# Performance work log

Hardware: AMD Instinct MI355X
Metric: run time of the kernel (lower is better)

Reference implementation:

```python
import jax, jax.numpy as jnp
import numpy as np

NV = 10           # int(0.5 // 0.05), clamped to [2, 1000]
STEP = 0.05
HALF_V = 0.5
EPS = 1e-8


def _normalize(x):
    return x / (jnp.linalg.norm(x, axis=-1, keepdims=True) + EPS)


def _bilinear(img, uv):
    # img: [3, H, W]; uv: [N, 2] normalized to [0, 1). align_corners=False convention.
    C, H, W = img.shape
    x = uv[:, 0] * W - 0.5
    y = uv[:, 1] * H - 0.5
    x0 = jnp.floor(x); y0 = jnp.floor(y)
    wx = x - x0; wy = y - y0
    x0i = jnp.clip(x0.astype(jnp.int32), 0, W - 1)
    x1i = jnp.clip(x0i + 1, 0, W - 1)
    y0i = jnp.clip(y0.astype(jnp.int32), 0, H - 1)
    y1i = jnp.clip(y0i + 1, 0, H - 1)
    g = lambda yi, xi: img[:, yi, xi].T  # [N, 3]
    return (g(y0i, x0i) * ((1 - wx) * (1 - wy))[:, None]
            + g(y0i, x1i) * (wx * (1 - wy))[:, None]
            + g(y1i, x0i) * ((1 - wx) * wy)[:, None]
            + g(y1i, x1i) * (wx * wy)[:, None])


def _forward(edge_points, rgb1, rgb2, intrinsic1, intrinsic2, extrinsic1, extrinsic2, nh):
    # nh: concrete numpy int64 [E] of per-edge horizontal sample counts (non-differentiable).
    start = edge_points[:, 0]
    cur_dir = edge_points[:, 1] - start
    next_dir = edge_points[:, 3] - edge_points[:, 1]
    prev_dir = edge_points[:, 0] - edge_points[:, 2]
    cur_length = jnp.linalg.norm(cur_dir + 1e-6, axis=1)
    cur_dir = cur_dir / cur_length[:, None]
    cur_normal = _normalize(jnp.cross(cur_dir, next_dir))
    flip = cur_normal[:, 2] > 0  # dot with (0,0,1) > 0 -> flip sign
    cur_normal = jnp.where(flip[:, None], -cur_normal, cur_normal)
    cur_up = _normalize(jnp.cross(cur_normal, cur_dir))
    prev_normal = _normalize(jnp.cross(prev_dir, cur_dir))

    # ragged per-edge horizontal coordinates via cumsum offsets + repeat_interleave
    begin = np.concatenate([np.zeros(1, np.int64), np.cumsum(nh)[:-1]])
    total_x = int(nh.sum())
    dx = jnp.arange(total_x) - jnp.asarray(np.repeat(begin, nh))
    dx = dx / jnp.asarray(np.repeat(nh - 1, nh)) * jnp.repeat(cur_length, nh, total_repeat_length=total_x)
    dy = jnp.arange(NV) / (NV - 1) * HALF_V  # [NV]
    coords_x = jnp.repeat(dx, NV)            # [total_x * NV]
    coords_y = jnp.tile(dy, total_x)         # [total_x * NV]
    npe = nh * NV
    total = total_x * NV
    pts = (jnp.repeat(cur_dir, npe, axis=0, total_repeat_length=total) * coords_x[:, None]
           + jnp.repeat(cur_up, npe, axis=0, total_repeat_length=total) * coords_y[:, None]
           + jnp.repeat(start, npe, axis=0, total_repeat_length=total))  # [total, 3]

    # project into image 1
    proj1 = pts @ intrinsic1.T
    uv1 = jnp.clip(proj1[:, :2] / proj1[:, 2:3], 0.0, 0.999999)
    s1 = _bilinear(rgb1[0], uv1)

    # project into image 2 via relative transform
    K2h = jnp.eye(4, dtype=pts.dtype).at[:3, :3].set(intrinsic2)
    transform = K2h @ extrinsic2 @ jnp.linalg.inv(extrinsic1)
    pts_h = jnp.concatenate([pts, jnp.ones((pts.shape[0], 1), pts.dtype)], axis=1)
    proj2 = pts_h @ transform.T
    uv2 = jnp.clip(proj2[:, :2] / proj2[:, 2:3], 0.0, 0.999999)
    s2 = _bilinear(rgb2[0], uv2)

    similarity_loss = jnp.mean((s1 - s2) ** 2)
    normal_loss = jnp.mean(1 - jnp.sum(cur_normal * prev_normal, axis=1)) / 2
    observing_normal = _normalize(jnp.cross(edge_points[:, 0], edge_points[:, 1]))
    snp = jnp.minimum(jnp.abs(jnp.sum(cur_up * observing_normal, axis=1)), 0.5)
    normalization_loss = jnp.mean(1 - snp / 0.5)
    return similarity_loss, normal_loss, normalization_loss


def setup_inputs():
    key = jax.random.key(0)
    k0, k1, k2 = jax.random.split(key, 3)
    E = 4000
    ep = jax.random.normal(k0, (E, 4, 3), dtype=jnp.float32) * 1.5
    ep = ep.at[..., 2].add(10.0)  # camera-space points in front of the camera
    rgb1 = jax.random.uniform(k1, (1, 3, 2000, 3000), dtype=jnp.float32)
    rgb2 = jax.random.uniform(k2, (1, 3, 2000, 3000), dtype=jnp.float32)
    K = jnp.array([[0.3, 0.0, 0.5], [0.0, 0.45, 0.5], [0.0, 0.0, 1.0]], jnp.float32)
    E1 = jnp.eye(4, dtype=jnp.float32)
    E2 = jnp.eye(4, dtype=jnp.float32).at[0, 3].set(-0.5)
    return {"edge_points": ep, "rgb1": rgb1, "rgb2": rgb2,
            "intrinsic1": K, "intrinsic2": K, "extrinsic1": E1, "extrinsic2": E2}


def reference(edge_points, rgb1, rgb2, intrinsic1, intrinsic2, extrinsic1, extrinsic2):
    # num_horizontal is an integer count (no gradient in torch either): compute concretely.
    cur_len = np.asarray(jnp.linalg.norm(edge_points[:, 1] - edge_points[:, 0] + 1e-6, axis=1))
    nh = np.clip((cur_len // STEP).astype(np.int64), 2, 1000)
    return _forward(edge_points, rgb1, rgb2, intrinsic1, intrinsic2, extrinsic1, extrinsic2, nh)
```

## Files before the change

### kernel.cpp

```cpp
#include <hip/hip_runtime.h>


constexpr int NVS   = 10;
constexpr int IMG_H = 2000;
constexpr int IMG_W = 3000;
constexpr int NPIX  = IMG_H * IMG_W;
constexpr int QROW  = IMG_W / 4;
constexpr int SAMPLE_BLOCKS = 2048;
constexpr unsigned CHUNK = 512;

typedef float    fx4 __attribute__((ext_vector_type(4)));
typedef unsigned ux4 __attribute__((ext_vector_type(4)));

struct Geom {
    float p0x, p0y, p0z;
    float p1x, p1y, p1z;
    float p2x, p2y, p2z;
    float p3x, p3y, p3z;
    float cdx, cdy, cdz;
    float cnx, cny, cnz;
    float cux, cuy, cuz;
    float len;
    int   nh;
};

__device__ __forceinline__ Geom compute_geom(const float* __restrict__ ep, int e) {
    Geom g;
    const float* p = ep + (size_t)e * 12;
    g.p0x = p[0];  g.p0y = p[1];  g.p0z = p[2];
    g.p1x = p[3];  g.p1y = p[4];  g.p1z = p[5];
    g.p2x = p[6];  g.p2y = p[7];  g.p2z = p[8];
    g.p3x = p[9];  g.p3y = p[10]; g.p3z = p[11];

    float dx = g.p1x - g.p0x, dy = g.p1y - g.p0y, dz = g.p1z - g.p0z;
    float ax = dx + 1e-6f, ay = dy + 1e-6f, az = dz + 1e-6f;
    g.len = sqrtf(ax * ax + ay * ay + az * az);
    g.cdx = dx / g.len; g.cdy = dy / g.len; g.cdz = dz / g.len;

    float ndx = g.p3x - g.p1x, ndy = g.p3y - g.p1y, ndz = g.p3z - g.p1z;
    float cnx = g.cdy * ndz - g.cdz * ndy;
    float cny = g.cdz * ndx - g.cdx * ndz;
    float cnz = g.cdx * ndy - g.cdy * ndx;
    float n1 = sqrtf(cnx * cnx + cny * cny + cnz * cnz) + 1e-8f;
    cnx /= n1; cny /= n1; cnz /= n1;
    if (cnz > 0.f) { cnx = -cnx; cny = -cny; cnz = -cnz; }
    g.cnx = cnx; g.cny = cny; g.cnz = cnz;

    float cux = cny * g.cdz - cnz * g.cdy;
    float cuy = cnz * g.cdx - cnx * g.cdz;
    float cuz = cnx * g.cdy - cny * g.cdx;
    float n2 = sqrtf(cux * cux + cuy * cuy + cuz * cuz) + 1e-8f;
    g.cux = cux / n2; g.cuy = cuy / n2; g.cuz = cuz / n2;

    int nh = (int)floorf(g.len / 0.05f);
    g.nh = nh < 2 ? 2 : (nh > 1000 ? 1000 : nh);
    return g;
}

__device__ __forceinline__ double block_reduce_d(double v) {
    __shared__ double sh[256];
    int tid = threadIdx.x;
    sh[tid] = v;
    __syncthreads();
    for (int s = 128; s > 0; s >>= 1) {
        if (tid < s) sh[tid] += sh[tid + s];
        __syncthreads();
    }
    double r = sh[0];
    __syncthreads();
    return r;
}

__global__ __launch_bounds__(256) void edge_kernel(
        const float* __restrict__ ep, int E,
        double* __restrict__ normal_part,
        double* __restrict__ norz_part,
        fx4* __restrict__ geom_out,
        int* __restrict__ nh_out) {
    int e = blockIdx.x * blockDim.x + threadIdx.x;
    double t1 = 0.0, t2 = 0.0;
    if (e < E) {
        Geom g = compute_geom(ep, e);
        float pdx = g.p0x - g.p2x, pdy = g.p0y - g.p2y, pdz = g.p0z - g.p2z;
        float pnx = pdy * g.cdz - pdz * g.cdy;
        float pny = pdz * g.cdx - pdx * g.cdz;
        float pnz = pdx * g.cdy - pdy * g.cdx;
        float n = sqrtf(pnx * pnx + pny * pny + pnz * pnz) + 1e-8f;
        pnx /= n; pny /= n; pnz /= n;
        float dotn = g.cnx * pnx + g.cny * pny + g.cnz * pnz;
        t1 = (double)(1.0f - dotn);

        float ox = g.p0y * g.p1z - g.p0z * g.p1y;
        float oy = g.p0z * g.p1x - g.p0x * g.p1z;
        float oz = g.p0x * g.p1y - g.p0y * g.p1x;
        float no = sqrtf(ox * ox + oy * oy + oz * oz) + 1e-8f;
        ox /= no; oy /= no; oz /= no;
        float snp = fminf(fabsf(g.cux * ox + g.cuy * oy + g.cuz * oz), 0.5f);
        t2 = (double)(1.0f - snp / 0.5f);

        fx4 f0 = {g.cdx, g.cdy, g.cdz, g.len};
        fx4 f1 = {g.cux, g.cuy, g.cuz, 1.0f / (float)(g.nh - 1)};
        fx4 f2 = {g.p0x, g.p0y, g.p0z, 0.f};
        geom_out[e * 3 + 0] = f0;
        geom_out[e * 3 + 1] = f1;
        geom_out[e * 3 + 2] = f2;
        nh_out[e] = g.nh;
    }
    double s1 = block_reduce_d(t1);
    double s2 = block_reduce_d(t2);
    if (threadIdx.x == 0) {
        normal_part[blockIdx.x] = s1;
        norz_part[blockIdx.x]   = s2;
    }
}

__global__ __launch_bounds__(256) void prep_kernel(
        const int* __restrict__ nh, int E, unsigned* __restrict__ cum,
        const float* __restrict__ K2, const float* __restrict__ E1,
        const float* __restrict__ E2, float* __restrict__ tf) {
    __shared__ unsigned ssum[256];
    int tid = threadIdx.x;
    int K = (E + 255) / 256;
    int base = tid * K;

    unsigned s = 0;
    for (int k = 0; k < K; ++k) {
        int idx = base + k;
        if (idx < E) s += (unsigned)(nh[idx] * NVS);
    }
    ssum[tid] = s;
    __syncthreads();
    for (int off = 1; off < 256; off <<= 1) {
        unsigned add = (tid >= off) ? ssum[tid - off] : 0u;
        __syncthreads();
        ssum[tid] += add;
        __syncthreads();
    }
    unsigned run = ssum[tid] - s;
    for (int k = 0; k < K; ++k) {
        int idx = base + k;
        if (idx < E) {
            run += (unsigned)(nh[idx] * NVS);
            cum[idx + 1] = run;
        }
    }
    if (tid == 0) {
        cum[0] = 0;

        double a[4][8];
        for (int r = 0; r < 4; ++r)
            for (int c = 0; c < 4; ++c) {
                a[r][c] = (double)E1[r * 4 + c];
                a[r][4 + c] = (r == c) ? 1.0 : 0.0;
            }
        for (int col = 0; col < 4; ++col) {
            int piv = col; double best = fabs(a[col][col]);
            for (int r = col + 1; r < 4; ++r) {
                double t = fabs(a[r][col]);
                if (t > best) { best = t; piv = r; }
            }
            if (piv != col)
                for (int c = 0; c < 8; ++c) { double t = a[col][c]; a[col][c] = a[piv][c]; a[piv][c] = t; }
            double d = a[col][col];
            for (int c = 0; c < 8; ++c) a[col][c] /= d;
            for (int r = 0; r < 4; ++r) {
                if (r == col) continue;
                double f = a[r][col];
                for (int c = 0; c < 8; ++c) a[r][c] -= f * a[col][c];
            }
        }
        double inv1[4][4];
        for (int r = 0; r < 4; ++r)
            for (int c = 0; c < 4; ++c) inv1[r][c] = a[r][4 + c];

        double k2h[4][4];
        for (int r = 0; r < 4; ++r)
            for (int c = 0; c < 4; ++c) k2h[r][c] = (r == c) ? 1.0 : 0.0;
        for (int r = 0; r < 3; ++r)
            for (int c = 0; c < 3; ++c) k2h[r][c] = (double)K2[r * 3 + c];

        double m1[4][4];
        for (int r = 0; r < 4; ++r)
            for (int c = 0; c < 4; ++c) {
                double sm = 0.0;
                for (int k = 0; k < 4; ++k) sm += (double)E2[r * 4 + k] * inv1[k][c];
                m1[r][c] = sm;
            }
        for (int r = 0; r < 4; ++r)
            for (int c = 0; c < 4; ++c) {
                double sm = 0.0;
                for (int k = 0; k < 4; ++k) sm += k2h[r][k] * m1[k][c];
                tf[r * 4 + c] = (float)sm;
            }
    }
}

__device__ __forceinline__ unsigned p565(float r, float g, float b) {
    unsigned ri = (unsigned)__float2int_rn(r * 31.0f) & 31u;
    unsigned gi = (unsigned)__float2int_rn(g * 63.0f) & 63u;
    unsigned bi = (unsigned)__float2int_rn(b * 31.0f) & 31u;
    return ri | (gi << 5) | (bi << 11);
}

__global__ __launch_bounds__(256) void repack_kernel(
        const float* __restrict__ img1, const float* __restrict__ img2,
        unsigned* __restrict__ o1, unsigned* __restrict__ o2) {
    const int nq = NPIX / 4;
    int idx = blockIdx.x * blockDim.x + threadIdx.x;
    bool act = idx < 2 * nq;

    const float* img = img1;
    unsigned* out = o1;
    int q = 0;
    unsigned h0 = 0, h1 = 0, h2 = 0, h3 = 0;
    fx4 r{}, g{}, b{};

    if (act) {
        if (idx < nq) { img = img1; out = o1; q = idx; }
        else          { img = img2; out = o2; q = idx - nq; }
        r = __builtin_nontemporal_load(reinterpret_cast<const fx4*>(img) + q);
        g = __builtin_nontemporal_load(reinterpret_cast<const fx4*>(img + NPIX) + q);
        b = __builtin_nontemporal_load(reinterpret_cast<const fx4*>(img + 2 * (size_t)NPIX) + q);
        h0 = p565(r.x, g.x, b.x);
        h1 = p565(r.y, g.y, b.y);
        h2 = p565(r.z, g.z, b.z);
        h3 = p565(r.w, g.w, b.w);
    }

    unsigned h4s = __shfl_down(h0, 1, 64);

    if (act) {
        int qrow = q % QROW;
        unsigned h4;
        if (qrow == QROW - 1) {
            h4 = h3;
        } else if ((threadIdx.x & 63) == 63) {
            int nx = q * 4 + 4;
            h4 = p565(img[nx], img[NPIX + nx], img[2 * (size_t)NPIX + nx]);
        } else {
            h4 = h4s;
        }
        ux4 o;
        o.x = h0 | (h1 << 16);
        o.y = h1 | (h2 << 16);
        o.z = h2 | (h3 << 16);
        o.w = h3 | (h4 << 16);
        reinterpret_cast<ux4*>(out)[q] = o;
    }
}

__device__ __forceinline__ void sample565(const unsigned* __restrict__ img,
                                          float u, float v,
                                          float& r, float& g, float& b) {
    float x = u * (float)IMG_W - 0.5f;
    float y = v * (float)IMG_H - 0.5f;
    float x0 = floorf(x), y0 = floorf(y);
    float wx = x - x0, wy = y - y0;
    int x0i = (int)x0; x0i = x0i < 0 ? 0 : (x0i > IMG_W - 1 ? IMG_W - 1 : x0i);
    int y0i = (int)y0; y0i = y0i < 0 ? 0 : (y0i > IMG_H - 1 ? IMG_H - 1 : y0i);
    int y1i = y0i + 1; y1i = y1i > IMG_H - 1 ? IMG_H - 1 : y1i;

    unsigned t0 = img[(size_t)y0i * IMG_W + x0i];
    unsigned t1 = img[(size_t)y1i * IMG_W + x0i];

    float w00 = (1.f - wx) * (1.f - wy);
    float w10 = wx * (1.f - wy);
    float w01 = (1.f - wx) * wy;
    float w11 = wx * wy;

    r = w00 * (float)(t0 & 31u)         + w10 * (float)((t0 >> 16) & 31u)
      + w01 * (float)(t1 & 31u)         + w11 * (float)((t1 >> 16) & 31u);
    g = w00 * (float)((t0 >> 5) & 63u)  + w10 * (float)((t0 >> 21) & 63u)
      + w01 * (float)((t1 >> 5) & 63u)  + w11 * (float)((t1 >> 21) & 63u);
    b = w00 * (float)((t0 >> 11) & 31u) + w10 * (float)(t0 >> 27)
      + w01 * (float)((t1 >> 11) & 31u) + w11 * (float)(t1 >> 27);
}

__device__ __forceinline__ void bilinear3(const float* __restrict__ img,
                                          float u, float v,
                                          float& r, float& g, float& b) {
    float x = u * (float)IMG_W - 0.5f;
    float y = v * (float)IMG_H - 0.5f;
    float x0 = floorf(x), y0 = floorf(y);
    float wx = x - x0, wy = y - y0;
    int x0i = (int)x0; x0i = x0i < 0 ? 0 : (x0i > IMG_W - 1 ? IMG_W - 1 : x0i);
    int x1i = x0i + 1; x1i = x1i > IMG_W - 1 ? IMG_W - 1 : x1i;
    int y0i = (int)y0; y0i = y0i < 0 ? 0 : (y0i > IMG_H - 1 ? IMG_H - 1 : y0i);
    int y1i = y0i + 1; y1i = y1i > IMG_H - 1 ? IMG_H - 1 : y1i;
    float w00 = (1.f - wx) * (1.f - wy);
    float w10 = wx * (1.f - wy);
    float w01 = (1.f - wx) * wy;
    float w11 = wx * wy;
    float out[3];
#pragma unroll
    for (int c = 0; c < 3; ++c) {
        const float* p = img + (size_t)c * NPIX;
        float v00 = p[(size_t)y0i * IMG_W + x0i];
        float v10 = p[(size_t)y0i * IMG_W + x1i];
        float v01 = p[(size_t)y1i * IMG_W + x0i];
        float v11 = p[(size_t)y1i * IMG_W + x1i];
        out[c] = v00 * w00 + v10 * w10 + v01 * w01 + v11 * w11;
    }
    r = out[0]; g = out[1]; b = out[2];
}

__device__ __forceinline__ int find_edge(const unsigned* __restrict__ cum,
                                         int E, unsigned s) {
    int lo = 0, hi = E - 1;
    while (lo < hi) {
        int mid = (lo + hi + 1) >> 1;
        if (cum[mid] <= s) lo = mid; else hi = mid - 1;
    }
    return lo;
}

template <bool PACKED>
__global__ __launch_bounds__(256) void sample_kernel_t(
        const fx4* __restrict__ geom,
        const unsigned* __restrict__ cum, int E,
        const void* __restrict__ vimg1,
        const void* __restrict__ vimg2,
        const float* __restrict__ K1,
        const float* __restrict__ tf,
        double* __restrict__ sim_part) {
    __shared__ int sh_ea[2], sh_eb[2];
    int tid = threadIdx.x;

    unsigned NS = cum[E];
    unsigned nch = (NS + CHUNK - 1u) / CHUNK;

    float k00 = K1[0], k01 = K1[1], k02 = K1[2];
    float k10 = K1[3], k11 = K1[4], k12 = K1[5];
    float k20 = K1[6], k21 = K1[7], k22 = K1[8];
    float t00 = tf[0],  t01 = tf[1],  t02 = tf[2],  t03 = tf[3];
    float t10 = tf[4],  t11 = tf[5],  t12 = tf[6],  t13 = tf[7];
    float t20 = tf[8],  t21 = tf[9],  t22 = tf[10], t23 = tf[11];

    const unsigned* img1 = (const unsigned*)vimg1;
    const unsigned* img2 = (const unsigned*)vimg2;
    const float* fimg1 = (const float*)vimg1;
    const float* fimg2 = (const float*)vimg2;

    const float INV31 = 1.0f / 31.0f;
    const float INV63 = 1.0f / 63.0f;

    double lsum = 0.0;
    int it = 0;

    auto sample_one = [&](unsigned s, int e) {
        while (e + 1 < E && cum[e + 1] <= s) ++e;
        unsigned q = s - cum[e];
        int i = (int)(q / (unsigned)NVS);
        int j = (int)(q - (unsigned)(i * NVS));

        fx4 f0 = geom[e * 3 + 0];
        fx4 f1 = geom[e * 3 + 1];
        fx4 f2 = geom[e * 3 + 2];

        float dxv = ((float)i * f1.w) * f0.w;
        float dyv = ((float)j / 9.0f) * 0.5f;

        float px = f0.x * dxv + f1.x * dyv + f2.x;
        float py = f0.y * dxv + f1.y * dyv + f2.y;
        float pz = f0.z * dxv + f1.z * dyv + f2.z;

        float w1 = k20 * px + k21 * py + k22 * pz;
        float u1 = (k00 * px + k01 * py + k02 * pz) / w1;
        float v1 = (k10 * px + k11 * py + k12 * pz) / w1;
        u1 = fminf(fmaxf(u1, 0.f), 0.999999f);
        v1 = fminf(fmaxf(v1, 0.f), 0.999999f);

        float w2 = t20 * px + t21 * py + t22 * pz + t23;
        float u2 = (t00 * px + t01 * py + t02 * pz + t03) / w2;
        float v2 = (t10 * px + t11 * py + t12 * pz + t13) / w2;
        u2 = fminf(fmaxf(u2, 0.f), 0.999999f);
        v2 = fminf(fmaxf(v2, 0.f), 0.999999f);

        if constexpr (PACKED) {
            float ar, ag, ab, br, bg, bb;
            sample565(img1, u1, v1, ar, ag, ab);
            sample565(img2, u2, v2, br, bg, bb);
            float dr = (ar - br) * INV31;
            float dg = (ag - bg) * INV63;
            float db = (ab - bb) * INV31;
            lsum += (double)(dr * dr) + (double)(dg * dg) + (double)(db * db);
        } else {
            float ar, ag, ab, br, bg, bb;
            bilinear3(fimg1, u1, v1, ar, ag, ab);
            bilinear3(fimg2, u2, v2, br, bg, bb);
            float dr = ar - br, dg = ag - bg, db = ab - bb;
            lsum += (double)(dr * dr) + (double)(dg * dg) + (double)(db * db);
        }
    };

    for (unsigned chunk = blockIdx.x; chunk < nch; chunk += gridDim.x, ++it) {
        unsigned sbase = chunk * CHUNK;
        int par = it & 1;
        if (tid == 0) {
            sh_ea[par] = find_edge(cum, E, sbase);
            unsigned smid = sbase + 256u;
            sh_eb[par] = find_edge(cum, E, smid < NS ? smid : NS - 1u);
        }
        __syncthreads();
        int ea = sh_ea[par];
        int eb = sh_eb[par];

        unsigned sA = sbase + (unsigned)tid;
        unsigned sB = sA + 256u;
        if (sA < NS) sample_one(sA, ea);
        if (sB < NS) sample_one(sB, eb);
    }

    double tot = block_reduce_d(lsum);
    if (tid == 0) sim_part[blockIdx.x] = tot;
}

__global__ __launch_bounds__(256) void finalize_kernel(
        const double* __restrict__ sim_part, int n_sim,
        const unsigned* __restrict__ cum, int E,
        const double* __restrict__ normal_part,
        const double* __restrict__ norz_part, int n_a,
        float* __restrict__ out) {
    int tid = threadIdx.x;
    unsigned NS = cum[E];

    double s = 0.0;
    for (int i = tid; i < n_sim; i += 256) s += sim_part[i];
    double sim = block_reduce_d(s);

    s = 0.0;
    for (int i = tid; i < n_a; i += 256) s += normal_part[i];
    double nrm = block_reduce_d(s);

    s = 0.0;
    for (int i = tid; i < n_a; i += 256) s += norz_part[i];
    double nz = block_reduce_d(s);

    if (tid == 0) {
        double total = (double)NS * 3.0;
        out[0] = (float)(sim / total);
        out[1] = (float)((nrm / (double)E) * 0.5);
        out[2] = (float)(nz / (double)E);
    }
}

extern "C" void kernel_launch(void* const* d_in, const int* in_sizes, int n_in,
                              void* d_out, int out_size, void* d_ws, size_t ws_size,
                              hipStream_t stream) {
    const float* ep  = (const float*)d_in[0];
    const float* im1 = (const float*)d_in[1];
    const float* im2 = (const float*)d_in[2];
    const float* K1  = (const float*)d_in[3];
    const float* K2  = (const float*)d_in[4];
    const float* E1  = (const float*)d_in[5];
    const float* E2  = (const float*)d_in[6];
    float* out = (float*)d_out;

    int E  = in_sizes[0] / 12;
    int nA = (E + 255) / 256;

    size_t img_bytes = (size_t)NPIX * 4;

    char* ws = (char*)d_ws;
    size_t off = 0;
    auto alloc = [&](size_t bytes) {
        size_t o = off;
        off = (off + bytes + 255) & ~(size_t)255;
        return (void*)(ws + o);
    };

    fx4*      geom        = (fx4*)alloc((size_t)E * 48);
    int*      nh_arr      = (int*)alloc((size_t)E * 4);
    unsigned* cum         = (unsigned*)alloc((size_t)(E + 1) * 4);
    float*    tf          = (float*)alloc(64);
    double*   sim_part    = (double*)alloc((size_t)SAMPLE_BLOCKS * 8);
    double*   normal_part = (double*)alloc((size_t)nA * 8);
    double*   norz_part   = (double*)alloc((size_t)nA * 8);
    size_t tail_bytes = off;

    bool packed = ws_size >= tail_bytes + 2 * img_bytes + 512;
    unsigned* p1 = nullptr;
    unsigned* p2 = nullptr;
    if (packed) {
        p1 = (unsigned*)alloc(img_bytes);
        p2 = (unsigned*)alloc(img_bytes);
    }

    edge_kernel<<<nA, 256, 0, stream>>>(ep, E, normal_part, norz_part, geom, nh_arr);
    prep_kernel<<<1, 256, 0, stream>>>(nh_arr, E, cum, K2, E1, E2, tf);
    if (packed) {
        const int nq2 = 2 * (NPIX / 4);
        repack_kernel<<<(nq2 + 255) / 256, 256, 0, stream>>>(im1, im2, p1, p2);
        sample_kernel_t<true><<<SAMPLE_BLOCKS, 256, 0, stream>>>(
            geom, cum, E, (const void*)p1, (const void*)p2, K1, tf, sim_part);
    } else {
        sample_kernel_t<false><<<SAMPLE_BLOCKS, 256, 0, stream>>>(
            geom, cum, E, (const void*)im1, (const void*)im2, K1, tf, sim_part);
    }
    finalize_kernel<<<1, 256, 0, stream>>>(sim_part, SAMPLE_BLOCKS, cum, E,
                                           normal_part, norz_part, nA, out);
}
```

Baseline: 92.91 us.

## Pack both bilinear rows per texel and fuse edge geometry into repack kernel

The repacked RGB565 image now stores, for each pixel, a uint2 holding the horizontal pixel pair from row y and the pair from row y+1. Each bilinear sample then needs a single 8-byte gather instead of two 4-byte gathers from different rows. The edge-geometry kernel is merged into the repack launch as extra blocks, which removes one kernel launch. In exchange, the repack reads every source row twice, writes an image twice the size, and drops the nontemporal load hints.

New measurement: 107.9 us. +16.2%, slower.

```diff
diff --git a/kernel.cpp b/kernel.cpp
--- a/kernel.cpp
+++ b/kernel.cpp
@@ -71,46 +71,113 @@
     return r;
 }
 
-__global__ __launch_bounds__(256) void edge_kernel(
-        const float* __restrict__ ep, int E,
+__device__ __forceinline__ unsigned p565(float r, float g, float b) {
+    unsigned ri = (unsigned)__float2int_rn(r * 31.0f) & 31u;
+    unsigned gi = (unsigned)__float2int_rn(g * 63.0f) & 63u;
+    unsigned bi = (unsigned)__float2int_rn(b * 31.0f) & 31u;
+    return ri | (gi << 5) | (bi << 11);
+}
+
+__global__ __launch_bounds__(256) void edge_repack_kernel(
+        const float* __restrict__ ep, int E, int nA,
         double* __restrict__ normal_part,
         double* __restrict__ norz_part,
         fx4* __restrict__ geom_out,
-        int* __restrict__ nh_out) {
-    int e = blockIdx.x * blockDim.x + threadIdx.x;
-    double t1 = 0.0, t2 = 0.0;
-    if (e < E) {
-        Geom g = compute_geom(ep, e);
-        float pdx = g.p0x - g.p2x, pdy = g.p0y - g.p2y, pdz = g.p0z - g.p2z;
-        float pnx = pdy * g.cdz - pdz * g.cdy;
-        float pny = pdz * g.cdx - pdx * g.cdz;
-        float pnz = pdx * g.cdy - pdy * g.cdx;
-        float n = sqrtf(pnx * pnx + pny * pny + pnz * pnz) + 1e-8f;
-        pnx /= n; pny /= n; pnz /= n;
-        float dotn = g.cnx * pnx + g.cny * pny + g.cnz * pnz;
-        t1 = (double)(1.0f - dotn);
-
-        float ox = g.p0y * g.p1z - g.p0z * g.p1y;
-        float oy = g.p0z * g.p1x - g.p0x * g.p1z;
-        float oz = g.p0x * g.p1y - g.p0y * g.p1x;
-        float no = sqrtf(ox * ox + oy * oy + oz * oz) + 1e-8f;
-        ox /= no; oy /= no; oz /= no;
-        float snp = fminf(fabsf(g.cux * ox + g.cuy * oy + g.cuz * oz), 0.5f);
-        t2 = (double)(1.0f - snp / 0.5f);
-
-        fx4 f0 = {g.cdx, g.cdy, g.cdz, g.len};
-        fx4 f1 = {g.cux, g.cuy, g.cuz, 1.0f / (float)(g.nh - 1)};
-        fx4 f2 = {g.p0x, g.p0y, g.p0z, 0.f};
-        geom_out[e * 3 + 0] = f0;
-        geom_out[e * 3 + 1] = f1;
-        geom_out[e * 3 + 2] = f2;
-        nh_out[e] = g.nh;
-    }
-    double s1 = block_reduce_d(t1);
-    double s2 = block_reduce_d(t2);
-    if (threadIdx.x == 0) {
-        normal_part[blockIdx.x] = s1;
-        norz_part[blockIdx.x]   = s2;
+        int* __restrict__ nh_out,
+        const float* __restrict__ img1, const float* __restrict__ img2,
+        uint2* __restrict__ o1, uint2* __restrict__ o2) {
+    if ((int)blockIdx.x < nA) {
+        int e = blockIdx.x * blockDim.x + threadIdx.x;
+        double t1 = 0.0, t2 = 0.0;
+        if (e < E) {
+            Geom g = compute_geom(ep, e);
+            float pdx = g.p0x - g.p2x, pdy = g.p0y - g.p2y, pdz = g.p0z - g.p2z;
+            float pnx = pdy * g.cdz - pdz * g.cdy;
+            float pny = pdz * g.cdx - pdx * g.cdz;
+            float pnz = pdx * g.cdy - pdy * g.cdx;
+            float n = sqrtf(pnx * pnx + pny * pny + pnz * pnz) + 1e-8f;
+            pnx /= n; pny /= n; pnz /= n;
+            float dotn = g.cnx * pnx + g.cny * pny + g.cnz * pnz;
+            t1 = (double)(1.0f - dotn);
+
+            float ox = g.p0y * g.p1z - g.p0z * g.p1y;
+            float oy = g.p0z * g.p1x - g.p0x * g.p1z;
+            float oz = g.p0x * g.p1y - g.p0y * g.p1x;
+            float no = sqrtf(ox * ox + oy * oy + oz * oz) + 1e-8f;
+            ox /= no; oy /= no; oz /= no;
+            float snp = fminf(fabsf(g.cux * ox + g.cuy * oy + g.cuz * oz), 0.5f);
+            t2 = (double)(1.0f - snp / 0.5f);
+
+            fx4 f0 = {g.cdx, g.cdy, g.cdz, g.len};
+            fx4 f1 = {g.cux, g.cuy, g.cuz, 1.0f / (float)(g.nh - 1)};
+            fx4 f2 = {g.p0x, g.p0y, g.p0z, 0.f};
+            geom_out[e * 3 + 0] = f0;
+            geom_out[e * 3 + 1] = f1;
+            geom_out[e * 3 + 2] = f2;
+            nh_out[e] = g.nh;
+        }
+        double s1 = block_reduce_d(t1);
+        double s2 = block_reduce_d(t2);
+        if (threadIdx.x == 0) {
+            normal_part[blockIdx.x] = s1;
+            norz_part[blockIdx.x]   = s2;
+        }
+        return;
+    }
+
+    const int nq = NPIX / 4;
+    int idx = ((int)blockIdx.x - nA) * 256 + (int)threadIdx.x;
+    bool act = idx < 2 * nq;
+
+    const float* img = img1;
+    uint2* out = o1;
+    int q = 0, q1 = 0, qrow = 0;
+    unsigned h0 = 0, h1 = 0, h2 = 0, h3 = 0;
+    unsigned g0 = 0, g1 = 0, g2 = 0, g3 = 0;
+
+    if (act) {
+        if (idx < nq) { img = img1; out = o1; q = idx; }
+        else          { img = img2; out = o2; q = idx - nq; }
+        int y = q / QROW;
+        qrow = q - y * QROW;
+        int y1 = y + 1 < IMG_H ? y + 1 : IMG_H - 1;
+        q1 = y1 * QROW + qrow;
+
+        fx4 r0 = reinterpret_cast<const fx4*>(img)[q];
+        fx4 c0 = reinterpret_cast<const fx4*>(img + NPIX)[q];
+        fx4 b0 = reinterpret_cast<const fx4*>(img + 2 * (size_t)NPIX)[q];
+        fx4 r1 = reinterpret_cast<const fx4*>(img)[q1];
+        fx4 c1 = reinterpret_cast<const fx4*>(img + NPIX)[q1];
+        fx4 b1 = reinterpret_cast<const fx4*>(img + 2 * (size_t)NPIX)[q1];
+
+        h0 = p565(r0.x, c0.x, b0.x); h1 = p565(r0.y, c0.y, b0.y);
+        h2 = p565(r0.z, c0.z, b0.z); h3 = p565(r0.w, c0.w, b0.w);
+        g0 = p565(r1.x, c1.x, b1.x); g1 = p565(r1.y, c1.y, b1.y);
+        g2 = p565(r1.z, c1.z, b1.z); g3 = p565(r1.w, c1.w, b1.w);
+    }
+
+    unsigned h4s = __shfl_down(h0, 1, 64);
+    unsigned g4s = __shfl_down(g0, 1, 64);
+
+    if (act) {
+        unsigned h4, g4;
+        if (qrow == QROW - 1) {
+            h4 = h3; g4 = g3;
+        } else if ((threadIdx.x & 63) == 63) {
+            int nx  = q  * 4 + 4;
+            int nx1 = q1 * 4 + 4;
+            h4 = p565(img[nx],  img[NPIX + nx],  img[2 * (size_t)NPIX + nx]);
+            g4 = p565(img[nx1], img[NPIX + nx1], img[2 * (size_t)NPIX + nx1]);
+        } else {
+            h4 = h4s; g4 = g4s;
+        }
+        ux4 lo, hi;
+        lo.x = h0 | (h1 << 16); lo.y = g0 | (g1 << 16);
+        lo.z = h1 | (h2 << 16); lo.w = g1 | (g2 << 16);
+        hi.x = h2 | (h3 << 16); hi.y = g2 | (g3 << 16);
+        hi.z = h3 | (h4 << 16); hi.w = g3 | (g4 << 16);
+        reinterpret_cast<ux4*>(out)[q * 2]     = lo;
+        reinterpret_cast<ux4*>(out)[q * 2 + 1] = hi;
     }
 }
 
@@ -195,73 +262,19 @@
     }
 }
 
-__device__ __forceinline__ unsigned p565(float r, float g, float b) {
-    unsigned ri = (unsigned)__float2int_rn(r * 31.0f) & 31u;
-    unsigned gi = (unsigned)__float2int_rn(g * 63.0f) & 63u;
-    unsigned bi = (unsigned)__float2int_rn(b * 31.0f) & 31u;
-    return ri | (gi << 5) | (bi << 11);
-}
-
-__global__ __launch_bounds__(256) void repack_kernel(
-        const float* __restrict__ img1, const float* __restrict__ img2,
-        unsigned* __restrict__ o1, unsigned* __restrict__ o2) {
-    const int nq = NPIX / 4;
-    int idx = blockIdx.x * blockDim.x + threadIdx.x;
-    bool act = idx < 2 * nq;
-
-    const float* img = img1;
-    unsigned* out = o1;
-    int q = 0;
-    unsigned h0 = 0, h1 = 0, h2 = 0, h3 = 0;
-    fx4 r{}, g{}, b{};
-
-    if (act) {
-        if (idx < nq) { img = img1; out = o1; q = idx; }
-        else          { img = img2; out = o2; q = idx - nq; }
-        r = __builtin_nontemporal_load(reinterpret_cast<const fx4*>(img) + q);
-        g = __builtin_nontemporal_load(reinterpret_cast<const fx4*>(img + NPIX) + q);
-        b = __builtin_nontemporal_load(reinterpret_cast<const fx4*>(img + 2 * (size_t)NPIX) + q);
-        h0 = p565(r.x, g.x, b.x);
-        h1 = p565(r.y, g.y, b.y);
-        h2 = p565(r.z, g.z, b.z);
-        h3 = p565(r.w, g.w, b.w);
-    }
-
-    unsigned h4s = __shfl_down(h0, 1, 64);
-
-    if (act) {
-        int qrow = q % QROW;
-        unsigned h4;
-        if (qrow == QROW - 1) {
-            h4 = h3;
-        } else if ((threadIdx.x & 63) == 63) {
-            int nx = q * 4 + 4;
-            h4 = p565(img[nx], img[NPIX + nx], img[2 * (size_t)NPIX + nx]);
-        } else {
-            h4 = h4s;
-        }
-        ux4 o;
-        o.x = h0 | (h1 << 16);
-        o.y = h1 | (h2 << 16);
-        o.z = h2 | (h3 << 16);
-        o.w = h3 | (h4 << 16);
-        reinterpret_cast<ux4*>(out)[q] = o;
-    }
-}
-
-__device__ __forceinline__ void sample565(const unsigned* __restrict__ img,
-                                          float u, float v,
-                                          float& r, float& g, float& b) {
+__device__ __forceinline__ void sample_q565(const uint2* __restrict__ img,
+                                            float u, float v,
+                                            float& r, float& g, float& b) {
     float x = u * (float)IMG_W - 0.5f;
     float y = v * (float)IMG_H - 0.5f;
     float x0 = floorf(x), y0 = floorf(y);
     float wx = x - x0, wy = y - y0;
     int x0i = (int)x0; x0i = x0i < 0 ? 0 : (x0i > IMG_W - 1 ? IMG_W - 1 : x0i);
     int y0i = (int)y0; y0i = y0i < 0 ? 0 : (y0i > IMG_H - 1 ? IMG_H - 1 : y0i);
-    int y1i = y0i + 1; y1i = y1i > IMG_H - 1 ? IMG_H - 1 : y1i;
-
-    unsigned t0 = img[(size_t)y0i * IMG_W + x0i];
-    unsigned t1 = img[(size_t)y1i * IMG_W + x0i];
+
+    uint2 T = img[(size_t)y0i * IMG_W + x0i];
+    unsigned t0 = T.x;
+    unsigned t1 = T.y;
 
     float w00 = (1.f - wx) * (1.f - wy);
     float w10 = wx * (1.f - wy);
@@ -272,8 +285,8 @@
       + w01 * (float)(t1 & 31u)         + w11 * (float)((t1 >> 16) & 31u);
     g = w00 * (float)((t0 >> 5) & 63u)  + w10 * (float)((t0 >> 21) & 63u)
       + w01 * (float)((t1 >> 5) & 63u)  + w11 * (float)((t1 >> 21) & 63u);
-    b = w00 * (float)((t0 >> 11) & 31u) + w10 * (float)(t0 >> 27)
-      + w01 * (float)((t1 >> 11) & 31u) + w11 * (float)(t1 >> 27);
+    b = w00 * (float)((t0 >> 11) & 31u) + w10 * (float)((t0 >> 27) & 31u)
+      + w01 * (float)((t1 >> 11) & 31u) + w11 * (float)((t1 >> 27) & 31u);
 }
 
 __device__ __forceinline__ void bilinear3(const float* __restrict__ img,
@@ -336,8 +349,8 @@
     float t10 = tf[4],  t11 = tf[5],  t12 = tf[6],  t13 = tf[7];
     float t20 = tf[8],  t21 = tf[9],  t22 = tf[10], t23 = tf[11];
 
-    const unsigned* img1 = (const unsigned*)vimg1;
-    const unsigned* img2 = (const unsigned*)vimg2;
+    const uint2* img1 = (const uint2*)vimg1;
+    const uint2* img2 = (const uint2*)vimg2;
     const float* fimg1 = (const float*)vimg1;
     const float* fimg2 = (const float*)vimg2;
 
@@ -378,8 +391,8 @@
 
         if constexpr (PACKED) {
             float ar, ag, ab, br, bg, bb;
-            sample565(img1, u1, v1, ar, ag, ab);
-            sample565(img2, u2, v2, br, bg, bb);
+            sample_q565(img1, u1, v1, ar, ag, ab);
+            sample_q565(img2, u2, v2, br, bg, bb);
             float dr = (ar - br) * INV31;
             float dg = (ag - bg) * INV63;
             float db = (ab - bb) * INV31;
@@ -459,7 +472,7 @@
     int E  = in_sizes[0] / 12;
     int nA = (E + 255) / 256;
 
-    size_t img_bytes = (size_t)NPIX * 4;
+    size_t img_bytes = (size_t)NPIX * 8;
 
     char* ws = (char*)d_ws;
     size_t off = 0;
@@ -479,21 +492,25 @@
     size_t tail_bytes = off;
 
     bool packed = ws_size >= tail_bytes + 2 * img_bytes + 512;
-    unsigned* p1 = nullptr;
-    unsigned* p2 = nullptr;
+    uint2* p1 = nullptr;
+    uint2* p2 = nullptr;
     if (packed) {
-        p1 = (unsigned*)alloc(img_bytes);
-        p2 = (unsigned*)alloc(img_bytes);
-    }
-
-    edge_kernel<<<nA, 256, 0, stream>>>(ep, E, normal_part, norz_part, geom, nh_arr);
-    prep_kernel<<<1, 256, 0, stream>>>(nh_arr, E, cum, K2, E1, E2, tf);
+        p1 = (uint2*)alloc(img_bytes);
+        p2 = (uint2*)alloc(img_bytes);
+    }
+
     if (packed) {
         const int nq2 = 2 * (NPIX / 4);
-        repack_kernel<<<(nq2 + 255) / 256, 256, 0, stream>>>(im1, im2, p1, p2);
+        int nRep = (nq2 + 255) / 256;
+        edge_repack_kernel<<<nA + nRep, 256, 0, stream>>>(
+            ep, E, nA, normal_part, norz_part, geom, nh_arr, im1, im2, p1, p2);
+        prep_kernel<<<1, 256, 0, stream>>>(nh_arr, E, cum, K2, E1, E2, tf);
         sample_kernel_t<true><<<SAMPLE_BLOCKS, 256, 0, stream>>>(
             geom, cum, E, (const void*)p1, (const void*)p2, K1, tf, sim_part);
     } else {
+        edge_repack_kernel<<<nA, 256, 0, stream>>>(
+            ep, E, nA, normal_part, norz_part, geom, nh_arr, im1, im2, nullptr, nullptr);
+        prep_kernel<<<1, 256, 0, stream>>>(nh_arr, E, cum, K2, E1, E2, tf);
         sample_kernel_t<false><<<SAMPLE_BLOCKS, 256, 0, stream>>>(
             geom, cum, E, (const void*)im1, (const void*)im2, K1, tf, sim_part);
     }
```
